# Performance work log

Hardware: AMD Instinct MI355X
Metric: run time of the kernel (lower is better)

The kernel has to match this reference:

```python
import jax, jax.numpy as jnp
import numpy as np

TAU = 1.0      # temperature for gumbel-softmax
EPS = 1e-12    # F.normalize eps


def _l2norm(v, axis):
    n = jnp.sqrt(jnp.sum(v * v, axis=axis, keepdims=True))
    return v / jnp.maximum(n, EPS)


def setup_inputs() -> dict:
    key = jax.random.key(0)
    k1, k2, k3, k4 = jax.random.split(key, 4)
    b, c, h, w, n = 8, 512, 64, 64, 1024
    x = jax.random.normal(k1, (b, c, h, w), dtype=jnp.float32)
    centers = jax.random.normal(k2, (n, c), dtype=jnp.float32)          # VQ codebook
    clusters = jax.random.normal(k3, (n, c), dtype=jnp.float32)         # ClusterLookup param
    gumbel_noise = jax.random.gumbel(k4, (b, n, h, w), dtype=jnp.float32)
    return {"x": x, "centers": centers, "clusters": clusters, "gumbel_noise": gumbel_noise}


def reference(x, centers, clusters, gumbel_noise):
    # similarity logits: [b, n, h, w]
    inner = jnp.einsum('bchw,nc->bnhw', x, centers)
    # hard gumbel-softmax (straight-through) over code dim
    y_soft = jax.nn.softmax((inner + gumbel_noise) / TAU, axis=1)
    idx = jnp.argmax(y_soft, axis=1)                                     # [b, h, w]
    y_hard = jax.nn.one_hot(idx, centers.shape[0], axis=1, dtype=y_soft.dtype)
    one_hot = y_hard - jax.lax.stop_gradient(y_soft) + y_soft            # [b, n, h, w]
    # quantized features: codebook lookup expressed as einsum
    z_q = jnp.einsum('bnhw,nd->bdhw', one_hot, centers)                  # [b, c, h, w]
    # ClusterLookup(z_q, alpha=None, is_direct=False)
    nf = _l2norm(z_q, axis=1)
    ncl = _l2norm(clusters, axis=1)
    ip = jnp.einsum('bchw,nc->bnhw', nf, ncl)                            # cluster logits
    preds = jnp.argmax(ip, axis=1)                                       # [b, h, w] int
    probs = jax.nn.one_hot(preds, clusters.shape[0], axis=1, dtype=ip.dtype)
    cluster_loss = -jnp.mean(jnp.sum(probs * ip, axis=1))
    return (cluster_loss, preds, ip, z_q)
```

## Files before the change

### kernel.cpp

```cpp
#include <hip/hip_runtime.h>
#include <math.h>

#define C 512
#define HW 4096
#define N 1024
#define NPIX 32768
#define MARGIN 2.0f
#define CAP 512

typedef short s16x8 __attribute__((ext_vector_type(8)));
typedef float f32x4 __attribute__((ext_vector_type(4)));

__device__ inline unsigned short f2bf(float f) {
    unsigned int u = __float_as_uint(f);
    return (unsigned short)((u + 0x7FFFu + ((u >> 16) & 1u)) >> 16);
}
__device__ inline unsigned int mono(float v) {
    unsigned int u = __float_as_uint(v);
    return (u & 0x80000000u) ? ~u : (u | 0x80000000u);
}
__device__ inline float unmono(unsigned int u) {
    unsigned int v = (u & 0x80000000u) ? (u & 0x7FFFFFFFu) : ~u;
    return __uint_as_float(v);
}

__global__ __launch_bounds__(64) void k_norms(const float* __restrict__ centers,
                                              const float* __restrict__ clusters,
                                              float* __restrict__ cnorm,
                                              float* __restrict__ clnorm) {
    int r = blockIdx.x;
    const float* src = (r < N) ? (centers + (size_t)r * C) : (clusters + (size_t)(r - N) * C);
    int lane = threadIdx.x;
    float s = 0.f;
    for (int k = lane; k < C; k += 64) { float v = src[k]; s += v * v; }
    #pragma unroll
    for (int m = 1; m < 64; m <<= 1) s += __shfl_xor(s, m, 64);
    if (lane == 0) {
        float nrm = sqrtf(s);
        if (nrm < 1e-12f) nrm = 1e-12f;
        if (r < N) cnorm[r] = nrm; else clnorm[r - N] = nrm;
    }
}

__global__ __launch_bounds__(256) void k_gemmM(const float* __restrict__ centers,
                                               const float* __restrict__ clusters,
                                               const float* __restrict__ cnorm,
                                               const float* __restrict__ clnorm,
                                               float* __restrict__ M) {
    __shared__ float as[32][68];
    __shared__ float bs[32][68];
    int tid = threadIdx.x;
    int tx = tid & 15, ty = tid >> 4;
    int i0 = blockIdx.x * 64, j0 = blockIdx.y * 64;
    int lrow = tid >> 2, lkq = (tid & 3) * 8;
    float acc[4][4] = {};
    for (int kc = 0; kc < C; kc += 32) {
        float4 a0 = *(const float4*)(centers + (size_t)(i0 + lrow) * C + kc + lkq);
        float4 a1 = *(const float4*)(centers + (size_t)(i0 + lrow) * C + kc + lkq + 4);
        float4 b0 = *(const float4*)(clusters + (size_t)(j0 + lrow) * C + kc + lkq);
        float4 b1 = *(const float4*)(clusters + (size_t)(j0 + lrow) * C + kc + lkq + 4);
        __syncthreads();
        as[lkq+0][lrow]=a0.x; as[lkq+1][lrow]=a0.y; as[lkq+2][lrow]=a0.z; as[lkq+3][lrow]=a0.w;
        as[lkq+4][lrow]=a1.x; as[lkq+5][lrow]=a1.y; as[lkq+6][lrow]=a1.z; as[lkq+7][lrow]=a1.w;
        bs[lkq+0][lrow]=b0.x; bs[lkq+1][lrow]=b0.y; bs[lkq+2][lrow]=b0.z; bs[lkq+3][lrow]=b0.w;
        bs[lkq+4][lrow]=b1.x; bs[lkq+5][lrow]=b1.y; bs[lkq+6][lrow]=b1.z; bs[lkq+7][lrow]=b1.w;
        __syncthreads();
        #pragma unroll
        for (int k = 0; k < 32; k += 4) {
            float av[4][4], bv[4][4];
            #pragma unroll
            for (int kk = 0; kk < 4; ++kk) {
                float4 ta = *(const float4*)&as[k+kk][tx*4];
                float4 tb = *(const float4*)&bs[k+kk][ty*4];
                av[kk][0]=ta.x; av[kk][1]=ta.y; av[kk][2]=ta.z; av[kk][3]=ta.w;
                bv[kk][0]=tb.x; bv[kk][1]=tb.y; bv[kk][2]=tb.z; bv[kk][3]=tb.w;
            }
            #pragma unroll
            for (int kk = 0; kk < 4; ++kk)
                #pragma unroll
                for (int ii = 0; ii < 4; ++ii)
                    #pragma unroll
                    for (int jj = 0; jj < 4; ++jj)
                        acc[ii][jj] = fmaf(av[kk][ii], bv[kk][jj], acc[ii][jj]);
        }
    }
    float rci[4], rcj[4];
    #pragma unroll
    for (int ii = 0; ii < 4; ++ii) rci[ii] = cnorm[i0 + tx*4 + ii];
    #pragma unroll
    for (int jj = 0; jj < 4; ++jj) rcj[jj] = clnorm[j0 + ty*4 + jj];
    #pragma unroll
    for (int ii = 0; ii < 4; ++ii)
        #pragma unroll
        for (int jj = 0; jj < 4; ++jj)
            M[(size_t)(i0 + tx*4 + ii) * N + (j0 + ty*4 + jj)] = acc[ii][jj] / (rci[ii] * rcj[jj]);
}

__global__ __launch_bounds__(256) void k_rowstat(const float* __restrict__ M,
                                                 float* __restrict__ rowmax,
                                                 int* __restrict__ rowarg) {
    __shared__ float sv[256];
    __shared__ int   sa[256];
    int i = blockIdx.x, tid = threadIdx.x;
    float bv = -INFINITY; int ba = 0;
    for (int j = tid; j < N; j += 256) {
        float v = M[(size_t)i * N + j];
        if (v > bv || (v == bv && j < ba)) { bv = v; ba = j; }
    }
    sv[tid] = bv; sa[tid] = ba;
    __syncthreads();
    for (int s = 128; s > 0; s >>= 1) {
        if (tid < s) {
            float v = sv[tid + s]; int a = sa[tid + s];
            if (v > sv[tid] || (v == sv[tid] && a < sa[tid])) { sv[tid] = v; sa[tid] = a; }
        }
        __syncthreads();
    }
    if (tid == 0) { rowmax[i] = sv[0]; rowarg[i] = sa[0]; }
}

__global__ __launch_bounds__(64) void k_cenfrag(const float* __restrict__ centers,
                                                unsigned short* __restrict__ cenB) {
    int f = blockIdx.x;
    int nt = f >> 4, kt = f & 15;
    int lane = threadIdx.x;
    int r = lane & 15, g = lane >> 4;
    const float* src = centers + (size_t)(nt * 16 + r) * C + kt * 32 + g * 4;
    float4 lo = *(const float4*)src;
    float4 hi = *(const float4*)(src + 16);
    union { unsigned short us[8]; uint4 q; } u;
    u.us[0]=f2bf(lo.x); u.us[1]=f2bf(lo.y); u.us[2]=f2bf(lo.z); u.us[3]=f2bf(lo.w);
    u.us[4]=f2bf(hi.x); u.us[5]=f2bf(hi.y); u.us[6]=f2bf(hi.z); u.us[7]=f2bf(hi.w);
    *(uint4*)(cenB + ((size_t)f * 64 + lane) * 8) = u.q;
}

__global__ __launch_bounds__(256, 2) void k_fused(const float* __restrict__ x,
                                                  const unsigned short* __restrict__ cenB,
                                                  const float* __restrict__ gumbel,
                                                  const float* __restrict__ centers,
                                                  int* __restrict__ idxb) {
    __shared__ float xs[C * 20];
    __shared__ unsigned int pmax[16];
    __shared__ unsigned long long pixkey[16];
    __shared__ unsigned int candlist[CAP];
    __shared__ int candcount;

    int tid = threadIdx.x;
    int lane = tid & 63, w = tid >> 6;
    int r = lane & 15, g = lane >> 4;

    int tile = (int)((blockIdx.x >> 3) | ((blockIdx.x & 7) << 8));
    int p0 = tile << 4;
    int b = p0 >> 12, hw0 = p0 & (HW - 1);

    if (tid < 16) { pmax[tid] = 0u; pixkey[tid] = 0ull; }
    if (tid == 0) candcount = 0;

    const float* xb = x + (size_t)b * C * HW + hw0;
    #pragma unroll
    for (int kk = 0; kk < 8; ++kk) {
        int k = kk * 64 + (tid >> 2);
        int q = (tid & 3) << 2;
        float4 v = *(const float4*)(xb + (size_t)k * HW + q);
        *(float4*)&xs[k * 20 + q] = v;
    }
    __syncthreads();

    s16x8 a[16];
    #pragma unroll
    for (int kt = 0; kt < 16; ++kt) {
        int kb = kt * 32 + g * 4;
        s16x8 t;
        #pragma unroll
        for (int e = 0; e < 4; ++e) {
            t[e]     = (short)f2bf(xs[(kb + e) * 20 + r]);
            t[4 + e] = (short)f2bf(xs[(kb + 16 + e) * 20 + r]);
        }
        a[kt] = t;
    }

    float keep[64];
    const float* grow = gumbel + ((size_t)b * N + r) * HW + hw0 + g * 4;
    #pragma unroll
    for (int nt = 0; nt < 16; ++nt) {
        int ntg = (w << 4) + nt;
        float4 gv = *(const float4*)(grow + (size_t)ntg * 16 * HW);
        f32x4 acc = {0.f, 0.f, 0.f, 0.f};
        #pragma unroll
        for (int kt = 0; kt < 16; ++kt) {
            s16x8 bf = *(const s16x8*)(cenB + (((size_t)ntg * 16 + kt) * 64 + lane) * 8);
            acc = __builtin_amdgcn_mfma_f32_16x16x32_bf16(a[kt], bf, acc, 0, 0, 0);
        }
        keep[nt * 4 + 0] = acc[0] + gv.x;
        keep[nt * 4 + 1] = acc[1] + gv.y;
        keep[nt * 4 + 2] = acc[2] + gv.z;
        keep[nt * 4 + 3] = acc[3] + gv.w;
    }

    float m4[4];
    #pragma unroll
    for (int j = 0; j < 4; ++j) {
        float m = keep[j];
        #pragma unroll
        for (int nt = 1; nt < 16; ++nt) m = fmaxf(m, keep[nt * 4 + j]);
        m4[j] = m;
    }
    #pragma unroll
    for (int s2 = 1; s2 < 16; s2 <<= 1)
        #pragma unroll
        for (int j = 0; j < 4; ++j) m4[j] = fmaxf(m4[j], __shfl_xor(m4[j], s2, 64));
    if (r == 0) {
        #pragma unroll
        for (int j = 0; j < 4; ++j) atomicMax(&pmax[g * 4 + j], mono(m4[j]));
    }
    __syncthreads();

    float thr[4];
    #pragma unroll
    for (int j = 0; j < 4; ++j) thr[j] = unmono(pmax[g * 4 + j]) - MARGIN;
    #pragma unroll
    for (int nt = 0; nt < 16; ++nt)
        #pragma unroll
        for (int j = 0; j < 4; ++j)
            if (keep[nt * 4 + j] >= thr[j]) {
                int n = (((w << 4) + nt) << 4) + r;
                int pos = atomicAdd(&candcount, 1);
                if (pos < CAP) candlist[pos] = (unsigned int)n | ((unsigned int)(g * 4 + j) << 12);
            }
    __syncthreads();

    int cc = candcount; if (cc > CAP) cc = CAP;
    for (int t = w; t < cc; t += 4) {
        unsigned int e = candlist[t];
        int n = (int)(e & 1023u), pl = (int)(e >> 12);
        float s = 0.f;
        #pragma unroll
        for (int mm = 0; mm < 8; ++mm) {
            int k = lane + (mm << 6);
            s = fmaf(xs[k * 20 + pl], centers[(size_t)n * C + k], s);
        }
        #pragma unroll
        for (int s2 = 1; s2 < 64; s2 <<= 1) s += __shfl_xor(s, s2, 64);
        float val = s + gumbel[((size_t)b * N + n) * HW + hw0 + pl];
        if (lane == 0) {
            unsigned long long key = ((unsigned long long)mono(val) << 32) | (unsigned int)(1023 - n);
            atomicMax(&pixkey[pl], key);
        }
    }
    __syncthreads();
    if (tid < 16) idxb[p0 + tid] = 1023 - (int)(unsigned int)(pixkey[tid] & 0xFFFFFFFFull);
}

__global__ __launch_bounds__(256) void k_preds(const int* __restrict__ idxb,
                                               const float* __restrict__ rowmax,
                                               const int* __restrict__ rowarg,
                                               float* __restrict__ preds_out,
                                               float* __restrict__ partial) {
    __shared__ float sv[256];
    int gid = blockIdx.x * 256 + threadIdx.x;
    int i = idxb[gid];
    preds_out[gid] = (float)rowarg[i];
    sv[threadIdx.x] = rowmax[i];
    __syncthreads();
    for (int s = 128; s > 0; s >>= 1) {
        if (threadIdx.x < s) sv[threadIdx.x] += sv[threadIdx.x + s];
        __syncthreads();
    }
    if (threadIdx.x == 0) partial[blockIdx.x] = sv[0];
}

__global__ __launch_bounds__(256) void k_gather(const float* __restrict__ src, int ncols,
                                                const int* __restrict__ idx,
                                                float* __restrict__ dst) {
    __shared__ float rows[64][65];
    int tile = blockIdx.x;
    int col0 = blockIdx.y * 64;
    int tid = threadIdx.x;
    int lane = tid & 63, w = tid >> 6;
    int b = tile >> 6, hw0 = (tile & 63) << 6;
    #pragma unroll
    for (int r8 = 0; r8 < 16; ++r8) {
        int r = w * 16 + r8;
        int row = idx[tile * 64 + r];
        rows[r][lane] = src[(size_t)row * ncols + col0 + lane];
    }
    __syncthreads();
    #pragma unroll
    for (int jj = 0; jj < 16; ++jj) {
        int j = col0 + w * 16 + jj;
        dst[((size_t)b * ncols + j) * HW + hw0 + lane] = rows[lane][w * 16 + jj];
    }
}

__global__ __launch_bounds__(128) void k_loss(const float* __restrict__ partial,
                                              float* __restrict__ out) {
    __shared__ float sv[128];
    sv[threadIdx.x] = partial[threadIdx.x];
    __syncthreads();
    for (int s = 64; s > 0; s >>= 1) {
        if (threadIdx.x < s) sv[threadIdx.x] += sv[threadIdx.x + s];
        __syncthreads();
    }
    if (threadIdx.x == 0) out[0] = -(sv[0] / 32768.0f);
}

extern "C" void kernel_launch(void* const* d_in, const int* in_sizes, int n_in,
                              void* d_out, int out_size, void* d_ws, size_t ws_size,
                              hipStream_t stream) {
    const float* x        = (const float*)d_in[0];
    const float* centers  = (const float*)d_in[1];
    const float* clusters = (const float*)d_in[2];
    const float* gumbel   = (const float*)d_in[3];
    float* out = (float*)d_out;

    char* w = (char*)d_ws;
    int*   idxb    = (int*)w;
    float* cnorm   = (float*)(w + 131072);
    float* clnorm  = cnorm + 1024;
    float* rowmax  = clnorm + 1024;
    int*   rowarg  = (int*)(rowmax + 1024);
    float* partial = (float*)(rowarg + 1024);
    float* M       = (float*)(w + 262144);
    unsigned short* cenB = (unsigned short*)(w + 4456448);

    float* out_loss  = out;
    float* out_preds = out + 1;
    float* out_ip    = out + 1 + 32768;
    float* out_zq    = out + 1 + 32768 + (size_t)N * NPIX;

    k_norms  <<<2048, 64, 0, stream>>>(centers, clusters, cnorm, clnorm);
    k_gemmM  <<<dim3(16, 16), 256, 0, stream>>>(centers, clusters, cnorm, clnorm, M);
    k_rowstat<<<1024, 256, 0, stream>>>(M, rowmax, rowarg);
    k_cenfrag<<<1024, 64, 0, stream>>>(centers, cenB);
    k_fused  <<<2048, 256, 0, stream>>>(x, cenB, gumbel, centers, idxb);
    k_preds  <<<128, 256, 0, stream>>>(idxb, rowmax, rowarg, out_preds, partial);
    k_gather <<<dim3(512, 16), 256, 0, stream>>>(M, N, idxb, out_ip);
    k_gather <<<dim3(512, 8),  256, 0, stream>>>(centers, C, idxb, out_zq);
    k_loss   <<<1, 128, 0, stream>>>(partial, out_loss);
}
```

Before: 279.2 us.

## Pack candidate logits as fp16, swizzle LDS tile, split MFMA chains, widen rescoring

The fused kernel now keeps its 64 per-lane logits as packed fp16 pairs and folds the running max into the MFMA loop, which cuts register pressure so occupancy can rise from 2 to 3 blocks per CU. The x tile in LDS moves to a pixel-major, XOR-swizzled layout, so A fragments are built from float4 reads instead of scalar strided loads. Each tile's 16-step MFMA chain is split across two accumulators to break the dependency chain. Exact rescoring now handles four candidates per wavefront at once with float4 loads and a 16-lane reduction. The risk is that fp16 rounding of logits can move candidates across the margin threshold, but the margin of 2 and the exact fp32 rescoring should absorb this.

```diff
diff --git a/kernel.cpp b/kernel.cpp
--- a/kernel.cpp
+++ b/kernel.cpp
@@ -15,6 +15,12 @@
     unsigned int u = __float_as_uint(f);
     return (unsigned short)((u + 0x7FFFu + ((u >> 16) & 1u)) >> 16);
 }
+__device__ inline float h2f(unsigned short u) {
+    _Float16 h; __builtin_memcpy(&h, &u, 2); return (float)h;
+}
+__device__ inline unsigned short f2h(float f) {
+    _Float16 h = (_Float16)f; unsigned short u; __builtin_memcpy(&u, &h, 2); return u;
+}
 __device__ inline unsigned int mono(float v) {
     unsigned int u = __float_as_uint(v);
     return (u & 0x80000000u) ? ~u : (u | 0x80000000u);
@@ -23,6 +29,7 @@
     unsigned int v = (u & 0x80000000u) ? (u & 0x7FFFFFFFu) : ~u;
     return __uint_as_float(v);
 }
+__device__ inline int xsw(int px, int G) { return px * 512 + ((G ^ (px & 7)) << 2); }
 
 __global__ __launch_bounds__(64) void k_norms(const float* __restrict__ centers,
                                               const float* __restrict__ clusters,
@@ -134,12 +141,12 @@
     *(uint4*)(cenB + ((size_t)f * 64 + lane) * 8) = u.q;
 }
 
-__global__ __launch_bounds__(256, 2) void k_fused(const float* __restrict__ x,
+__global__ __launch_bounds__(256, 3) void k_fused(const float* __restrict__ x,
                                                   const unsigned short* __restrict__ cenB,
                                                   const float* __restrict__ gumbel,
                                                   const float* __restrict__ centers,
                                                   int* __restrict__ idxb) {
-    __shared__ float xs[C * 20];
+    __shared__ float xs[C * 16];
     __shared__ unsigned int pmax[16];
     __shared__ unsigned long long pixkey[16];
     __shared__ unsigned int candlist[CAP];
@@ -157,54 +164,61 @@
     if (tid == 0) candcount = 0;
 
     const float* xb = x + (size_t)b * C * HW + hw0;
-    #pragma unroll
-    for (int kk = 0; kk < 8; ++kk) {
-        int k = kk * 64 + (tid >> 2);
-        int q = (tid & 3) << 2;
-        float4 v = *(const float4*)(xb + (size_t)k * HW + q);
-        *(float4*)&xs[k * 20 + q] = v;
+    {
+        int k0 = tid >> 2, q = (tid & 3) << 2;
+        #pragma unroll
+        for (int kk = 0; kk < 8; ++kk) {
+            int k = kk * 64 + k0;
+            float4 v = *(const float4*)(xb + (size_t)k * HW + q);
+            int G = k >> 2, e = k & 3;
+            xs[xsw(q + 0, G) + e] = v.x;
+            xs[xsw(q + 1, G) + e] = v.y;
+            xs[xsw(q + 2, G) + e] = v.z;
+            xs[xsw(q + 3, G) + e] = v.w;
+        }
     }
     __syncthreads();
 
     s16x8 a[16];
     #pragma unroll
     for (int kt = 0; kt < 16; ++kt) {
-        int kb = kt * 32 + g * 4;
+        float4 lo = *(const float4*)&xs[xsw(r, kt * 8 + g)];
+        float4 hi = *(const float4*)&xs[xsw(r, kt * 8 + g + 4)];
         s16x8 t;
-        #pragma unroll
-        for (int e = 0; e < 4; ++e) {
-            t[e]     = (short)f2bf(xs[(kb + e) * 20 + r]);
-            t[4 + e] = (short)f2bf(xs[(kb + 16 + e) * 20 + r]);
-        }
+        t[0] = (short)f2bf(lo.x); t[1] = (short)f2bf(lo.y);
+        t[2] = (short)f2bf(lo.z); t[3] = (short)f2bf(lo.w);
+        t[4] = (short)f2bf(hi.x); t[5] = (short)f2bf(hi.y);
+        t[6] = (short)f2bf(hi.z); t[7] = (short)f2bf(hi.w);
         a[kt] = t;
     }
 
-    float keep[64];
+    unsigned int keepH[32];
+    float m4[4] = {-INFINITY, -INFINITY, -INFINITY, -INFINITY};
     const float* grow = gumbel + ((size_t)b * N + r) * HW + hw0 + g * 4;
     #pragma unroll
     for (int nt = 0; nt < 16; ++nt) {
         int ntg = (w << 4) + nt;
+        const unsigned short* bp = cenB + (size_t)ntg * 16 * 512 + lane * 8;
         float4 gv = *(const float4*)(grow + (size_t)ntg * 16 * HW);
-        f32x4 acc = {0.f, 0.f, 0.f, 0.f};
-        #pragma unroll
-        for (int kt = 0; kt < 16; ++kt) {
-            s16x8 bf = *(const s16x8*)(cenB + (((size_t)ntg * 16 + kt) * 64 + lane) * 8);
-            acc = __builtin_amdgcn_mfma_f32_16x16x32_bf16(a[kt], bf, acc, 0, 0, 0);
-        }
-        keep[nt * 4 + 0] = acc[0] + gv.x;
-        keep[nt * 4 + 1] = acc[1] + gv.y;
-        keep[nt * 4 + 2] = acc[2] + gv.z;
-        keep[nt * 4 + 3] = acc[3] + gv.w;
-    }
-
-    float m4[4];
-    #pragma unroll
-    for (int j = 0; j < 4; ++j) {
-        float m = keep[j];
-        #pragma unroll
-        for (int nt = 1; nt < 16; ++nt) m = fmaxf(m, keep[nt * 4 + j]);
-        m4[j] = m;
-    }
+        f32x4 acc0 = {0.f, 0.f, 0.f, 0.f};
+        f32x4 acc1 = {0.f, 0.f, 0.f, 0.f};
+        #pragma unroll
+        for (int kt = 0; kt < 16; kt += 2) {
+            s16x8 b0 = *(const s16x8*)(bp + (size_t)kt * 512);
+            s16x8 b1 = *(const s16x8*)(bp + (size_t)(kt + 1) * 512);
+            acc0 = __builtin_amdgcn_mfma_f32_16x16x32_bf16(a[kt],     b0, acc0, 0, 0, 0);
+            acc1 = __builtin_amdgcn_mfma_f32_16x16x32_bf16(a[kt + 1], b1, acc1, 0, 0, 0);
+        }
+        float v0 = acc0[0] + acc1[0] + gv.x;
+        float v1 = acc0[1] + acc1[1] + gv.y;
+        float v2 = acc0[2] + acc1[2] + gv.z;
+        float v3 = acc0[3] + acc1[3] + gv.w;
+        m4[0] = fmaxf(m4[0], v0); m4[1] = fmaxf(m4[1], v1);
+        m4[2] = fmaxf(m4[2], v2); m4[3] = fmaxf(m4[3], v3);
+        keepH[nt * 2]     = (unsigned int)f2h(v0) | ((unsigned int)f2h(v1) << 16);
+        keepH[nt * 2 + 1] = (unsigned int)f2h(v2) | ((unsigned int)f2h(v3) << 16);
+    }
+
     #pragma unroll
     for (int s2 = 1; s2 < 16; s2 <<= 1)
         #pragma unroll
@@ -219,30 +233,47 @@
     #pragma unroll
     for (int j = 0; j < 4; ++j) thr[j] = unmono(pmax[g * 4 + j]) - MARGIN;
     #pragma unroll
-    for (int nt = 0; nt < 16; ++nt)
-        #pragma unroll
-        for (int j = 0; j < 4; ++j)
-            if (keep[nt * 4 + j] >= thr[j]) {
-                int n = (((w << 4) + nt) << 4) + r;
+    for (int nt = 0; nt < 16; ++nt) {
+        int n0 = (((w << 4) + nt) << 4) + r;
+        #pragma unroll
+        for (int j2 = 0; j2 < 2; ++j2) {
+            unsigned int pk = keepH[nt * 2 + j2];
+            float lo = h2f((unsigned short)(pk & 0xFFFFu));
+            float hi = h2f((unsigned short)(pk >> 16));
+            int j = j2 * 2;
+            if (lo >= thr[j]) {
                 int pos = atomicAdd(&candcount, 1);
-                if (pos < CAP) candlist[pos] = (unsigned int)n | ((unsigned int)(g * 4 + j) << 12);
+                if (pos < CAP) candlist[pos] = (unsigned int)n0 | ((unsigned int)(g * 4 + j) << 12);
             }
+            if (hi >= thr[j + 1]) {
+                int pos = atomicAdd(&candcount, 1);
+                if (pos < CAP) candlist[pos] = (unsigned int)n0 | ((unsigned int)(g * 4 + j + 1) << 12);
+            }
+        }
+    }
     __syncthreads();
 
     int cc = candcount; if (cc > CAP) cc = CAP;
-    for (int t = w; t < cc; t += 4) {
-        unsigned int e = candlist[t];
+    int sl = lane & 15, cg = lane >> 4;
+    for (int t0 = w * 4; t0 < cc; t0 += 16) {
+        int c = t0 + cg;
+        bool valid = c < cc;
+        unsigned int e = candlist[valid ? c : 0];
         int n = (int)(e & 1023u), pl = (int)(e >> 12);
+        const float* cen = centers + (size_t)n * C;
         float s = 0.f;
         #pragma unroll
-        for (int mm = 0; mm < 8; ++mm) {
-            int k = lane + (mm << 6);
-            s = fmaf(xs[k * 20 + pl], centers[(size_t)n * C + k], s);
-        }
-        #pragma unroll
-        for (int s2 = 1; s2 < 64; s2 <<= 1) s += __shfl_xor(s, s2, 64);
-        float val = s + gumbel[((size_t)b * N + n) * HW + hw0 + pl];
-        if (lane == 0) {
+        for (int m = 0; m < 8; ++m) {
+            int G = sl + (m << 4);
+            float4 xv = *(const float4*)&xs[xsw(pl, G)];
+            float4 cv = *(const float4*)(cen + (G << 2));
+            s = fmaf(xv.x, cv.x, s); s = fmaf(xv.y, cv.y, s);
+            s = fmaf(xv.z, cv.z, s); s = fmaf(xv.w, cv.w, s);
+        }
+        #pragma unroll
+        for (int s2 = 1; s2 < 16; s2 <<= 1) s += __shfl_xor(s, s2, 64);
+        if (valid && sl == 0) {
+            float val = s + gumbel[((size_t)b * N + n) * HW + hw0 + pl];
             unsigned long long key = ((unsigned long long)mono(val) << 32) | (unsigned int)(1023 - n);
             atomicMax(&pixkey[pl], key);
         }
```

New measurement: 288.2 us. 1.03x slower.
